# Kernel optimization log

Hardware: AMD Instinct MI355X
Metric: run time of the kernel (lower is better)

Reference implementation:

```python
import jax, jax.numpy as jnp
import numpy as np

B = 4096          # effective_batch_size (world_size=1)
D = 128           # embedding_dim
T = 0.5           # temperature
CW = 0.5          # confidence_weight
PT = 0.8          # positive_threshold (cosine)


def setup_inputs() -> dict:
    key = jax.random.key(0)
    emb = jax.random.normal(key, (B, D), dtype=jnp.float32)
    emb = emb / jnp.linalg.norm(emb, axis=1, keepdims=True)  # cosine-sim embeddings
    return {"embedding": emb}


def reference(embedding):
    b = embedding.shape[0]
    half = b // 2
    idx = jnp.arange(b)
    pos_idx = (idx + half) % b  # positive pair index (other augmented view)

    # exp(sim / T), [B, B]
    sim = jnp.exp(embedding @ embedding.T / T)

    # precomputed masks (world_size=1, rank=0, num_pos=2):
    # positive mask: the other view; negative mask: everything except self and its pair
    pos_mask = jnp.zeros((b, b), dtype=sim.dtype).at[idx, pos_idx].set(1.0)
    neg_mask = 1.0 - pos_mask - jnp.eye(b, dtype=sim.dtype)

    all_pos = sim * pos_mask
    all_neg = sim * neg_mask

    pos_sim = sim[idx, pos_idx]  # [B]

    # diff_sim: |sim - pos_sim| on upper triangle (j >= i), 3 elsewhere,
    # with diagonal and (i, i+half) for i < half also set to 3
    upper = idx[None, :] >= idx[:, None]
    excl = jnp.eye(b, dtype=bool) | ((idx[:, None] < half) & (idx[None, :] == idx[:, None] + half))
    diff_sim = jnp.where(upper & ~excl, jnp.abs(sim - pos_sim[:, None]), jnp.asarray(3.0, sim.dtype))

    # all argmin locations (torch.where(diff_sim == min)) -> boolean select mask
    min_mask = diff_sim == jnp.min(diff_sim)
    conf = (jnp.log(pos_sim) * T >= PT)[:, None]  # per-anchor confidence gate
    sel = min_mask & conf

    # false-negative reweighting (pos read of all_neg happens before neg update)
    new_pos = jnp.where(sel & (all_pos == 0.0), CW * all_neg, all_pos)
    new_neg = jnp.where(sel & (all_neg != 0.0), (1.0 - CW) * all_neg, all_neg)

    pos = jnp.sum(new_pos, axis=1)
    neg = jnp.sum(new_neg, axis=1)
    return -jnp.mean(jnp.log(pos / (pos + neg)))
```

## Files before the change

kernel.cpp:

```cpp
#include <hip/hip_runtime.h>
#include <hip/hip_bf16.h>
#include <math.h>

#define B_N  4096
#define HALF 2048
#define D_K  128
#define TI   128
#define TJ   64
#define NTI  32
#define NTJ  64
#define JPB  4
#define NJG  (NTJ / JPB)

typedef __attribute__((ext_vector_type(8))) short bf16x8;
typedef __attribute__((ext_vector_type(4))) float f32x4;

__device__ __forceinline__ ushort f2bf(float x) {
    unsigned u = __float_as_uint(x);
    unsigned r = u + 0x7FFFu + ((u >> 16) & 1u);
    return (ushort)(r >> 16);
}

__device__ __forceinline__ void gload_lds16(const ushort* g, ushort* l) {
    __builtin_amdgcn_global_load_lds(
        (const __attribute__((address_space(1))) unsigned int*)g,
        (__attribute__((address_space(3))) unsigned int*)l, 16, 0, 0);
}

__device__ __forceinline__ bf16x8 read_fragB(const ushort* lds, int row, int kbyte) {
    int byte = ((row << 8) | kbyte) ^ ((row & 7) << 4);
    return *(const bf16x8*)((const char*)lds + byte);
}

__global__ __launch_bounds__(256) void k0_prep(const float* __restrict__ emb,
                                               ushort* __restrict__ embh,
                                               float* __restrict__ pos_sim,
                                               float* __restrict__ conf,
                                               float* __restrict__ neg_acc,
                                               float* __restrict__ corrpart,
                                               unsigned* __restrict__ counter) {
    int tid = threadIdx.x;
    int gtid = blockIdx.x * 256 + tid;
    float4 v = ((const float4*)emb)[gtid];
    ushort4 h;
    h.x = f2bf(v.x); h.y = f2bf(v.y); h.z = f2bf(v.z); h.w = f2bf(v.w);
    ((ushort4*)embh)[gtid] = h;
    ((float2*)corrpart)[gtid] = make_float2(0.f, 0.f);

    if (blockIdx.x < 256) {
        int r   = blockIdx.x * 16 + (tid >> 4);
        int l16 = tid & 15;
        const float* a = emb + (size_t)r * D_K + l16 * 8;
        const float* b = emb + (size_t)(r ^ HALF) * D_K + l16 * 8;
        float4 x0 = *(const float4*)a, x1 = *(const float4*)(a + 4);
        float4 y0 = *(const float4*)b, y1 = *(const float4*)(b + 4);
        float d = 0.f;
        d = fmaf(x0.x, y0.x, d); d = fmaf(x0.y, y0.y, d);
        d = fmaf(x0.z, y0.z, d); d = fmaf(x0.w, y0.w, d);
        d = fmaf(x1.x, y1.x, d); d = fmaf(x1.y, y1.y, d);
        d = fmaf(x1.z, y1.z, d); d = fmaf(x1.w, y1.w, d);
#pragma unroll
        for (int off = 1; off < 16; off <<= 1) d += __shfl_xor(d, off);
        if (l16 == 0) {
            float ps = expf(d * 2.0f);
            pos_sim[r] = ps;
            conf[r]    = (logf(ps) * 0.5f >= 0.8f) ? 1.0f : 0.0f;
            neg_acc[r] = 0.f;
        }
    }
    if (gtid == 0) *counter = 0u;
}

__global__ __launch_bounds__(256, 3) void k1_main(const ushort* __restrict__ embh,
                                                  const float* __restrict__ pos_sim,
                                                  const float* __restrict__ conf,
                                                  float* __restrict__ neg_acc,
                                                  float* __restrict__ corrpart,
                                                  unsigned* __restrict__ tile_min) {
    int bi = blockIdx.y, jg = blockIdx.x;
    __shared__ ushort B0[TJ * D_K];
    __shared__ ushort B1[TJ * D_K];

    int tid = threadIdx.x, lane = tid & 63, wr = tid >> 6;
    int l15 = lane & 15;
    int k8  = (lane >> 4) << 3;
    int jr4 = (lane >> 4) << 2;

    {
        const ushort* srcB = embh + (size_t)(jg * JPB) * TJ * D_K;
#pragma unroll
        for (int it = 0; it < 4; ++it) {
            int f = tid + 256 * it;
            int r = f >> 4, c = f & 15;
            int g = (r << 4) | (c ^ (r & 7));
            gload_lds16(srcB + g * 8, B0 + f * 8);
        }
    }

    int I0 = bi * TI + wr * 32;
    bf16x8 A0[4], A1[4];
    {
        const ushort* a0 = embh + (size_t)(I0 + l15) * D_K + k8;
        const ushort* a1 = embh + (size_t)(I0 + 16 + l15) * D_K + k8;
#pragma unroll
        for (int ks = 0; ks < 4; ++ks) {
            A0[ks] = *(const bf16x8*)(a0 + ks * 32);
            A1[ks] = *(const bf16x8*)(a1 + ks * 32);
        }
    }

    int jtd = I0 >> 6;
    float psi0 = pos_sim[I0 + l15];
    float psi1 = pos_sim[I0 + 16 + l15];
    float cf0  = conf[I0 + l15];
    float cf1  = conf[I0 + 16 + l15];
    bool anyc  = __any((cf0 != 0.f) || (cf1 != 0.f));
    float negacc0 = 0.f, negacc1 = 0.f;

    __syncthreads();

#pragma unroll
    for (int t = 0; t < JPB; ++t) {
        const ushort* Bc = (t & 1) ? B1 : B0;
        ushort*       Bn = (t & 1) ? B0 : B1;
        int jt = jg * JPB + t;

        if (t + 1 < JPB) {
            const ushort* srcB = embh + (size_t)(jt + 1) * TJ * D_K;
#pragma unroll
            for (int it = 0; it < 4; ++it) {
                int f = tid + 256 * it;
                int r = f >> 4, c = f & 15;
                int g = (r << 4) | (c ^ (r & 7));
                gload_lds16(srcB + g * 8, Bn + f * 8);
            }
        }

        f32x4 acc[2][4];
#pragma unroll
        for (int m = 0; m < 2; ++m)
#pragma unroll
            for (int n = 0; n < 4; ++n) acc[m][n] = (f32x4){0.f, 0.f, 0.f, 0.f};
#pragma unroll
        for (int ks = 0; ks < 4; ++ks) {
            int kb = ks * 64 + (k8 << 1);
            bf16x8 b[4];
#pragma unroll
            for (int n = 0; n < 4; ++n) b[n] = read_fragB(Bc, l15 + n * 16, kb);
#pragma unroll
            for (int n = 0; n < 4; ++n) {
                acc[0][n] = __builtin_amdgcn_mfma_f32_16x16x32_bf16(b[n], A0[ks], acc[0][n], 0, 0, 0);
                acc[1][n] = __builtin_amdgcn_mfma_f32_16x16x32_bf16(b[n], A1[ks], acc[1][n], 0, 0, 0);
            }
        }
#pragma unroll
        for (int m = 0; m < 2; ++m)
#pragma unroll
            for (int n = 0; n < 4; ++n)
#pragma unroll
                for (int reg = 0; reg < 4; ++reg)
                    acc[m][n][reg] = __expf(acc[m][n][reg] * 2.0f);

        int j0 = jt * TJ;
        bool mixed = (jt == jtd), postt = (jt == (jtd ^ 32)), upT = (jt > jtd);
        float tmin = 3.0f;
#pragma unroll
        for (int m = 0; m < 2; ++m) {
            int i = I0 + m * 16 + l15;
            float psi = m ? psi1 : psi0;
            float np = 0.f;
            if (mixed) {
#pragma unroll
                for (int n = 0; n < 4; ++n)
#pragma unroll
                    for (int reg = 0; reg < 4; ++reg) {
                        float s = acc[m][n][reg];
                        int j = j0 + n * 16 + jr4 + reg;
                        if (j != i) np += s;
                        if (j > i)  tmin = fminf(tmin, fabsf(s - psi));
                    }
            } else if (postt) {
                int pidx = i ^ HALF;
#pragma unroll
                for (int n = 0; n < 4; ++n)
#pragma unroll
                    for (int reg = 0; reg < 4; ++reg) {
                        float s = acc[m][n][reg];
                        int j = j0 + n * 16 + jr4 + reg;
                        if (j != pidx) {
                            np += s;
                            if (upT) tmin = fminf(tmin, fabsf(s - psi));
                        }
                    }
            } else {
                float l0 = 3.f, l1 = 3.f, l2 = 3.f, l3 = 3.f;
#pragma unroll
                for (int n = 0; n < 4; ++n) {
                    float s0 = acc[m][n][0], s1 = acc[m][n][1];
                    float s2 = acc[m][n][2], s3 = acc[m][n][3];
                    np += (s0 + s1) + (s2 + s3);
                    if (upT) {
                        l0 = fminf(l0, fabsf(s0 - psi)); l1 = fminf(l1, fabsf(s1 - psi));
                        l2 = fminf(l2, fabsf(s2 - psi)); l3 = fminf(l3, fabsf(s3 - psi));
                    }
                }
                tmin = fminf(tmin, fminf(fminf(l0, l1), fminf(l2, l3)));
            }
            if (m) negacc1 += np; else negacc0 += np;
        }
#pragma unroll
        for (int off = 32; off; off >>= 1)
            tmin = fminf(tmin, __shfl_xor(tmin, off));
        if (lane == 0)
            tile_min[(bi * 4 + wr) * NTJ + jt] = __float_as_uint(tmin);

        if (anyc) {
#pragma unroll
            for (int m = 0; m < 2; ++m) {
                int i = I0 + m * 16 + l15;
                float psi = m ? psi1 : psi0;
                bool ci = ((m ? cf1 : cf0) != 0.f);
                float corr = 0.f;
#pragma unroll
                for (int n = 0; n < 4; ++n)
#pragma unroll
                    for (int reg = 0; reg < 4; ++reg) {
                        float s = acc[m][n][reg];
                        int j = j0 + n * 16 + jr4 + reg;
                        float d = 3.0f;
                        if (mixed)      { if (j > i) d = fabsf(s - psi); }
                        else if (postt) { if (upT && j != (i ^ HALF)) d = fabsf(s - psi); }
                        else if (upT)   d = fabsf(s - psi);
                        if (ci && d == tmin) corr += 0.5f * s;
                    }
                corr += __shfl_xor(corr, 16);
                corr += __shfl_xor(corr, 32);
                if (lane < 16) corrpart[(size_t)jt * B_N + i] = corr;
            }
        }
        if (t + 1 < JPB) __syncthreads();
    }

    negacc0 += __shfl_xor(negacc0, 16);
    negacc0 += __shfl_xor(negacc0, 32);
    negacc1 += __shfl_xor(negacc1, 16);
    negacc1 += __shfl_xor(negacc1, 32);
    if (lane < 16) {
        atomicAdd(&neg_acc[I0 + lane],      negacc0);
        atomicAdd(&neg_acc[I0 + 16 + lane], negacc1);
    }
}

__global__ __launch_bounds__(128) void k3_loss(const float* __restrict__ pos_sim,
                                               const float* __restrict__ neg_acc,
                                               const float* __restrict__ corrpart,
                                               const unsigned* __restrict__ tile_min,
                                               float* __restrict__ partial,
                                               unsigned* __restrict__ counter,
                                               float* __restrict__ out) {
    int t = threadIdx.x, bi = blockIdx.x;
    unsigned gmv = 0xFFFFFFFFu;
#pragma unroll
    for (int k = 0; k < 64; ++k) gmv = min(gmv, tile_min[t + 128 * k]);
#pragma unroll
    for (int off = 32; off; off >>= 1) {
        unsigned o = (unsigned)__shfl_xor((int)gmv, off);
        gmv = min(gmv, o);
    }
    __shared__ unsigned gred[2];
    if ((t & 63) == 0) gred[t >> 6] = gmv;
    __syncthreads();
    unsigned gm = min(gred[0], gred[1]);

    int i = bi * 128 + t;
    int si = i >> 5;
    float corr = 0.f;
#pragma unroll 8
    for (int jt = 0; jt < NTJ; ++jt)
        if (tile_min[si * NTJ + jt] == gm)
            corr += corrpart[(size_t)jt * B_N + i];
    float pos = pos_sim[i] + corr;
    float neg = neg_acc[i] - corr;
    float l = logf(pos / (pos + neg));
#pragma unroll
    for (int off = 32; off; off >>= 1) l += __shfl_xor(l, off);
    __shared__ float w2[2];
    if ((t & 63) == 0) w2[t >> 6] = l;
    __syncthreads();
    if (t == 0) {
        partial[bi] = w2[0] + w2[1];
        __threadfence();
        unsigned c = atomicAdd(counter, 1u);
        if (c == NTI - 1) {
            __threadfence();
            float tot = 0.f;
            volatile float* vp = partial;
            for (int b = 0; b < NTI; ++b) tot += vp[b];
            *out = -tot / (float)B_N;
        }
    }
}

extern "C" void kernel_launch(void* const* d_in, const int* in_sizes, int n_in,
                              void* d_out, int out_size, void* d_ws, size_t ws_size,
                              hipStream_t stream) {
    const float* emb = (const float*)d_in[0];
    float* out = (float*)d_out;

    char* ws = (char*)d_ws;
    ushort*   embh      = (ushort*)ws;
    float*    fbase     = (float*)(ws + 1048576);
    float*    pos_sim   = fbase;
    float*    conf      = fbase + 4096;
    float*    neg_acc   = fbase + 8192;
    float*    corrpart  = fbase + 12288;
    float*    partial   = corrpart + (size_t)NTJ * B_N;
    unsigned* tile_min  = (unsigned*)(partial + 32);
    unsigned* counter   = tile_min + 128 * NTJ;

    k0_prep<<<512, 256, 0, stream>>>(emb, embh, pos_sim, conf, neg_acc,
                                     corrpart, counter);
    k1_main<<<dim3(NJG, NTI), 256, 0, stream>>>(embh, pos_sim, conf, neg_acc,
                                                corrpart, tile_min);
    k3_loss<<<NTI, 128, 0, stream>>>(pos_sim, neg_acc, corrpart, tile_min,
                                     partial, counter, out);
}
```

Measured before the change: 33.02 us.

## Drop corrpart zero-fill from prep, batch tile-min reductions and stores

The prep kernel no longer zero-fills the large corrpart buffer. Instead, the main kernel writes zeros only for row tiles with no confident anchors. The positive-pair dot product is now computed by every thread, using a second float4 load of the paired row, which removes the branch and the extra per-row loads. Tile-min wavefront reductions are deferred and batched across the four j-tiles, with one grouped store at the end. The reduction is done early only where the correction path needs it. This trades a full-buffer memset for a conditional write and reorders the reduction work.

```diff
diff --git a/kernel.cpp b/kernel.cpp
--- a/kernel.cpp
+++ b/kernel.cpp
@@ -37,36 +37,24 @@
                                                float* __restrict__ pos_sim,
                                                float* __restrict__ conf,
                                                float* __restrict__ neg_acc,
-                                               float* __restrict__ corrpart,
                                                unsigned* __restrict__ counter) {
-    int tid = threadIdx.x;
-    int gtid = blockIdx.x * 256 + tid;
+    int gtid = blockIdx.x * 256 + threadIdx.x;
     float4 v = ((const float4*)emb)[gtid];
+    float4 p = ((const float4*)emb)[gtid ^ 65536];
     ushort4 h;
     h.x = f2bf(v.x); h.y = f2bf(v.y); h.z = f2bf(v.z); h.w = f2bf(v.w);
     ((ushort4*)embh)[gtid] = h;
-    ((float2*)corrpart)[gtid] = make_float2(0.f, 0.f);
-
-    if (blockIdx.x < 256) {
-        int r   = blockIdx.x * 16 + (tid >> 4);
-        int l16 = tid & 15;
-        const float* a = emb + (size_t)r * D_K + l16 * 8;
-        const float* b = emb + (size_t)(r ^ HALF) * D_K + l16 * 8;
-        float4 x0 = *(const float4*)a, x1 = *(const float4*)(a + 4);
-        float4 y0 = *(const float4*)b, y1 = *(const float4*)(b + 4);
-        float d = 0.f;
-        d = fmaf(x0.x, y0.x, d); d = fmaf(x0.y, y0.y, d);
-        d = fmaf(x0.z, y0.z, d); d = fmaf(x0.w, y0.w, d);
-        d = fmaf(x1.x, y1.x, d); d = fmaf(x1.y, y1.y, d);
-        d = fmaf(x1.z, y1.z, d); d = fmaf(x1.w, y1.w, d);
-#pragma unroll
-        for (int off = 1; off < 16; off <<= 1) d += __shfl_xor(d, off);
-        if (l16 == 0) {
-            float ps = expf(d * 2.0f);
-            pos_sim[r] = ps;
-            conf[r]    = (logf(ps) * 0.5f >= 0.8f) ? 1.0f : 0.0f;
-            neg_acc[r] = 0.f;
-        }
+    float d = 0.f;
+    d = fmaf(v.x, p.x, d); d = fmaf(v.y, p.y, d);
+    d = fmaf(v.z, p.z, d); d = fmaf(v.w, p.w, d);
+#pragma unroll
+    for (int off = 1; off < 32; off <<= 1) d += __shfl_xor(d, off);
+    if ((gtid & 31) == 0) {
+        int r = gtid >> 5;
+        float ps = expf(d * 2.0f);
+        pos_sim[r] = ps;
+        conf[r]    = (logf(ps) * 0.5f >= 0.8f) ? 1.0f : 0.0f;
+        neg_acc[r] = 0.f;
     }
     if (gtid == 0) *counter = 0u;
 }
@@ -116,6 +104,7 @@
     float cf1  = conf[I0 + 16 + l15];
     bool anyc  = __any((cf0 != 0.f) || (cf1 != 0.f));
     float negacc0 = 0.f, negacc1 = 0.f;
+    float tl[JPB];
 
     __syncthreads();
 
@@ -208,13 +197,14 @@
             }
             if (m) negacc1 += np; else negacc0 += np;
         }
-#pragma unroll
-        for (int off = 32; off; off >>= 1)
-            tmin = fminf(tmin, __shfl_xor(tmin, off));
-        if (lane == 0)
-            tile_min[(bi * 4 + wr) * NTJ + jt] = __float_as_uint(tmin);
+        tl[t] = tmin;
 
         if (anyc) {
+            float wt = tmin;
+#pragma unroll
+            for (int off = 32; off; off >>= 1)
+                wt = fminf(wt, __shfl_xor(wt, off));
+            tl[t] = wt;
 #pragma unroll
             for (int m = 0; m < 2; ++m) {
                 int i = I0 + m * 16 + l15;
@@ -231,7 +221,7 @@
                         if (mixed)      { if (j > i) d = fabsf(s - psi); }
                         else if (postt) { if (upT && j != (i ^ HALF)) d = fabsf(s - psi); }
                         else if (upT)   d = fabsf(s - psi);
-                        if (ci && d == tmin) corr += 0.5f * s;
+                        if (ci && d == wt) corr += 0.5f * s;
                     }
                 corr += __shfl_xor(corr, 16);
                 corr += __shfl_xor(corr, 32);
@@ -239,6 +229,28 @@
             }
         }
         if (t + 1 < JPB) __syncthreads();
+    }
+
+#pragma unroll
+    for (int off = 32; off; off >>= 1) {
+#pragma unroll
+        for (int t = 0; t < JPB; ++t)
+            tl[t] = fminf(tl[t], __shfl_xor(tl[t], off));
+    }
+    if (lane == 0) {
+        int base = (bi * 4 + wr) * NTJ + jg * JPB;
+        tile_min[base + 0] = __float_as_uint(tl[0]);
+        tile_min[base + 1] = __float_as_uint(tl[1]);
+        tile_min[base + 2] = __float_as_uint(tl[2]);
+        tile_min[base + 3] = __float_as_uint(tl[3]);
+    }
+
+    if (!anyc && lane < 16) {
+#pragma unroll
+        for (int t = 0; t < JPB; ++t) {
+            corrpart[(size_t)(jg * JPB + t) * B_N + I0 + lane]      = 0.f;
+            corrpart[(size_t)(jg * JPB + t) * B_N + I0 + 16 + lane] = 0.f;
+        }
     }
 
     negacc0 += __shfl_xor(negacc0, 16);
@@ -318,8 +330,7 @@
     unsigned* tile_min  = (unsigned*)(partial + 32);
     unsigned* counter   = tile_min + 128 * NTJ;
 
-    k0_prep<<<512, 256, 0, stream>>>(emb, embh, pos_sim, conf, neg_acc,
-                                     corrpart, counter);
+    k0_prep<<<512, 256, 0, stream>>>(emb, embh, pos_sim, conf, neg_acc, counter);
     k1_main<<<dim3(NJG, NTI), 256, 0, stream>>>(embh, pos_sim, conf, neg_acc,
                                                 corrpart, tile_min);
     k3_loss<<<NTI, 128, 0, stream>>>(pos_sim, neg_acc, corrpart, tile_min,
```

Result: no change. 32.62 us (-1.2%).
